# Kernel tuning notes

Measured on AMD Instinct MI355X. Metric: run time of the kernel, lower is better.

The kernel has to match this reference:

```python
import jax, jax.numpy as jnp
import numpy as np

N = 100000   # total nodes (batched molecules)
E = 250000   # directed edges
B = 2000     # number of graphs
F_IN = 75    # atom feature dim
DIM = 32     # hidden dim


def setup_inputs() -> dict:
    key = jax.random.key(0)
    ks = jax.random.split(key, 12)
    def gl(k, shape, fan_in):
        return (jax.random.normal(k, shape, jnp.float32) / np.sqrt(fan_in)).astype(jnp.float32)
    inp = {}
    inp['node_features'] = jax.random.normal(ks[0], (N, F_IN), jnp.float32)
    inp['edge_features'] = jax.random.normal(ks[1], (E, 11), jnp.float32)
    inp['lin0_w'] = gl(ks[2], (DIM, F_IN), F_IN)
    inp['lin0_b'] = jnp.zeros((DIM,), jnp.float32)
    # edge network: Linear(11,128) -> ReLU -> Linear(128, DIM*DIM)
    inp['nn_w1'] = gl(ks[3], (128, 11), 11)
    inp['nn_b1'] = jnp.zeros((128,), jnp.float32)
    inp['nn_w2'] = gl(ks[4], (DIM * DIM, 128), 128)
    inp['nn_b2'] = jnp.zeros((DIM * DIM,), jnp.float32)
    inp['conv_bias'] = jnp.zeros((DIM,), jnp.float32)  # NNConv bias (root_weight=False)
    # GRU(dim, dim), torch gate order: r, z, n
    inp['gru_wih'] = gl(ks[5], (3 * DIM, DIM), DIM)
    inp['gru_whh'] = gl(ks[6], (3 * DIM, DIM), DIM)
    inp['gru_bih'] = jnp.zeros((3 * DIM,), jnp.float32)
    inp['gru_bhh'] = jnp.zeros((3 * DIM,), jnp.float32)
    # Set2Set LSTM(2*dim, dim), torch gate order: i, f, g, o
    inp['lstm_wih'] = gl(ks[7], (4 * DIM, 2 * DIM), 2 * DIM)
    inp['lstm_whh'] = gl(ks[8], (4 * DIM, DIM), DIM)
    inp['lstm_bih'] = jnp.zeros((4 * DIM,), jnp.float32)
    inp['lstm_bhh'] = jnp.zeros((4 * DIM,), jnp.float32)
    inp['edge_index'] = jax.random.randint(ks[9], (2, E), 0, N)
    inp['graph_index'] = jnp.sort(jax.random.randint(ks[10], (N,), 0, B))
    return inp


def _nnconv(x, edge_w, src, dst, bias):
    # per-edge: gather src features, apply [dim,dim] edge weight, scatter-mean to dst
    msg = jnp.einsum('ei,eio->eo', x[src], edge_w)           # [E, DIM]
    s = jax.ops.segment_sum(msg, dst, num_segments=N)         # [N, DIM]
    cnt = jax.ops.segment_sum(jnp.ones((msg.shape[0],), msg.dtype), dst, num_segments=N)
    mean = s / jnp.maximum(cnt, 1.0)[:, None]
    return mean + bias


def _gru_cell(x, h, wih, whh, bih, bhh):
    gi = x @ wih.T + bih
    gh = h @ whh.T + bhh
    gi_r, gi_z, gi_n = jnp.split(gi, 3, axis=-1)
    gh_r, gh_z, gh_n = jnp.split(gh, 3, axis=-1)
    r = jax.nn.sigmoid(gi_r + gh_r)
    z = jax.nn.sigmoid(gi_z + gh_z)
    n = jnp.tanh(gi_n + r * gh_n)
    return (1.0 - z) * n + z * h


def _lstm_cell(x, h, c, wih, whh, bih, bhh):
    g = x @ wih.T + bih + h @ whh.T + bhh
    i, f, gg, o = jnp.split(g, 4, axis=-1)
    c = jax.nn.sigmoid(f) * c + jax.nn.sigmoid(i) * jnp.tanh(gg)
    h = jax.nn.sigmoid(o) * jnp.tanh(c)
    return h, c


def _set2set(x, batch, wih, whh, bih, bhh, steps=3):
    dim = x.shape[-1]
    h = jnp.zeros((B, dim), x.dtype)
    c = jnp.zeros((B, dim), x.dtype)
    q_star = jnp.zeros((B, 2 * dim), x.dtype)
    for _ in range(steps):
        q, c = _lstm_cell(q_star, h, c, wih, whh, bih, bhh)
        h = q
        e = jnp.sum(x * q[batch], axis=-1)                    # [N]
        emax = jax.ops.segment_max(e, batch, num_segments=B)
        ex = jnp.exp(e - emax[batch])
        denom = jax.ops.segment_sum(ex, batch, num_segments=B)
        a = ex / denom[batch]
        r = jax.ops.segment_sum(a[:, None] * x, batch, num_segments=B)
        q_star = jnp.concatenate([q, r], axis=-1)
    return q_star


def reference(node_features, edge_features, lin0_w, lin0_b, nn_w1, nn_b1, nn_w2, nn_b2,
              conv_bias, gru_wih, gru_whh, gru_bih, gru_bhh,
              lstm_wih, lstm_whh, lstm_bih, lstm_bhh, edge_index, graph_index):
    src, dst = edge_index[0], edge_index[1]
    out = jax.nn.relu(node_features @ lin0_w.T + lin0_b)      # [N, DIM]
    # edge network (edge_features are fixed -> identical every iteration)
    hw = jax.nn.relu(edge_features @ nn_w1.T + nn_b1)
    edge_w = (hw @ nn_w2.T + nn_b2).reshape(-1, DIM, DIM)     # [E, DIM, DIM]
    h = out
    for _ in range(3):
        m = jax.nn.relu(_nnconv(out, edge_w, src, dst, conv_bias))
        h = _gru_cell(m, h, gru_wih, gru_whh, gru_bih, gru_bhh)
        out = h
    pooled = _set2set(out, graph_index, lstm_wih, lstm_whh, lstm_bih, lstm_bhh)
    return pooled, out
```

## Files before the change

### kernel.cpp

```cpp
#include <hip/hip_runtime.h>
#include <stdint.h>

#define N_NODES  100000
#define N_EDGES  250000
#define N_GRAPHS 2000
#define F_IN     75
#define DIM      32
#define H1       128

#define MSG_BLOCKS 977
#define CH        8
#define NSTAGES   17
#define KT_PAD    (CH * NSTAGES)
#define W2F_HALFS (KT_PAD * 1024)

#define CNT_BLOCKS  ((N_EDGES + 255) / 256)
#define OFFS_BLOCKS ((N_NODES + 255) / 256)
#define GRUW_BLOCKS 32

typedef _Float16 v8h __attribute__((ext_vector_type(8)));
typedef float    v4f __attribute__((ext_vector_type(4)));

__device__ __forceinline__ void gld_lds16(const void* g, void* l) {
    __builtin_amdgcn_global_load_lds(
        (const __attribute__((address_space(1))) unsigned int*)g,
        (__attribute__((address_space(3))) unsigned int*)l, 16, 0, 0);
}

__global__ __launch_bounds__(256) void lin0_kernel(
    const float* __restrict__ nf, const float* __restrict__ w,
    const float* __restrict__ b, _Float16* __restrict__ h16) {
    __shared__ float wl[DIM * F_IN];
    __shared__ float bl[DIM];
    int t = threadIdx.x;
    for (int i = t; i < DIM * F_IN; i += 256) wl[i] = w[i];
    if (t < DIM) bl[t] = b[t];
    __syncthreads();
    int nl = t >> 5, o = t & 31;
    #pragma unroll
    for (int p = 0; p < 4; ++p) {
        int n = blockIdx.x * 32 + p * 8 + nl;
        if (n >= N_NODES) continue;
        const float* row = nf + (size_t)n * F_IN;
        float acc = bl[o];
        #pragma unroll
        for (int i = 0; i < F_IN; ++i) acc += row[i] * wl[o * F_IN + i];
        h16[(size_t)n * DIM + o] = (_Float16)fmaxf(acc, 0.f);
    }
}

__global__ __launch_bounds__(256) void prep_w2f_kernel(
    const float* __restrict__ w2, const float* __restrict__ b2,
    _Float16* __restrict__ w2f) {
    int id = blockIdx.x * 256 + threadIdx.x;
    if (id >= W2F_HALFS) return;
    int j    = id & 7;
    int lane = (id >> 3) & 63;
    int ng   = (id >> 9) & 1;
    int kt   = id >> 10;
    int lr = lane & 15, q = lane >> 4;
    int c = kt * 32 + q * 8 + j;
    int o = ng * 16 + lr;
    float val = 0.f;
    if (c < 4096)      val = w2[((c >> 7) * 32 + o) * H1 + (c & 127)];
    else if (c < 4128) val = b2[(c - 4096) * 32 + o];
    w2f[id] = (_Float16)val;
}

__global__ __launch_bounds__(256) void hw_kernel(
    const float* __restrict__ ef, const float* __restrict__ w1,
    const float* __restrict__ b1, _Float16* __restrict__ hwf,
    int e_off) {
    __shared__ float wl[H1 * 11];
    __shared__ float bl[H1];
    int t = threadIdx.x;
    for (int i = t; i < H1 * 11; i += 256) wl[i] = w1[i];
    if (t < H1) bl[t] = b1[t];
    __syncthreads();
    int k = t & 127;
    #pragma unroll
    for (int p = 0; p < 16; ++p) {
        int le = blockIdx.x * 32 + p * 2 + (t >> 7);
        int e  = e_off + le;
        float acc = 0.f;
        if (e < N_EDGES) {
            const float* row = ef + (size_t)e * 11;
            acc = bl[k];
            #pragma unroll
            for (int i = 0; i < 11; ++i) acc += row[i] * wl[k * 11 + i];
            acc = fmaxf(acc, 0.f);
        }
        size_t addr = (size_t)(le >> 4) * 2048 + (k >> 3) * 128 + (le & 15) * 8 + (k & 7);
        hwf[addr] = (_Float16)acc;
    }
}

__global__ __launch_bounds__(256) void aux_kernel(
    const int* __restrict__ dst, float* __restrict__ cnt,
    const int* __restrict__ gidx, int* __restrict__ gstart,
    const float* __restrict__ wih, const float* __restrict__ whh,
    _Float16* __restrict__ gw) {
    int t = threadIdx.x;
    if (blockIdx.x < CNT_BLOCKS) {
        int e = blockIdx.x * 256 + t;
        if (e < N_EDGES) atomicAdd(&cnt[dst[e]], 1.0f);
    } else if (blockIdx.x < CNT_BLOCKS + OFFS_BLOCKS) {
        int n = (blockIdx.x - CNT_BLOCKS) * 256 + t;
        if (n >= N_NODES) return;
        int b = gidx[n];
        if (n == 0) {
            for (int bb = 0; bb <= b; ++bb) gstart[bb] = 0;
        } else {
            int a = gidx[n - 1];
            for (int bb = a + 1; bb <= b; ++bb) gstart[bb] = n;
        }
        if (n == N_NODES - 1) {
            for (int bb = b + 1; bb <= N_GRAPHS; ++bb) gstart[bb] = N_NODES;
        }
    } else {
        int id = (blockIdx.x - CNT_BLOCKS - OFFS_BLOCKS) * 256 + t;
        if (id >= 8192) return;
        int im = id & 4095;
        int r = im / 40, c = im - r * 40;
        float val = 0.f;
        if (r < 96 && c < 32) val = (id < 4096) ? wih[r * 32 + c] : whh[r * 32 + c];
        gw[id] = (_Float16)val;
    }
}

__global__ __launch_bounds__(256) void msg_kernel(
    const _Float16* __restrict__ hwf, const _Float16* __restrict__ w2f,
    const _Float16* __restrict__ x16, const int* __restrict__ src,
    const int* __restrict__ dst, float* __restrict__ sbuf, int e_off) {
    __shared__ _Float16 xs[32 * 256];
    __shared__ _Float16 bst[2][CH * 1024];

    int t = threadIdx.x;
    int w = t >> 6, lane = t & 63, lr = lane & 15, q = lane >> 4;
    int wbase = w * 64;

    {
        const char* gp = (const char*)w2f;
        char* lp = (char*)&bst[0][0];
        #pragma unroll
        for (int it = 0; it < 4; ++it)
            gld_lds16(gp + it * 4096 + t * 16, lp + it * 4096 + t * 16);
    }

    v8h hwr[4][4];
    {
        const v8h* hv = (const v8h*)hwf;
        int T0 = blockIdx.x * 16 + w * 4;
        #pragma unroll
        for (int mt = 0; mt < 4; ++mt)
            #pragma unroll
            for (int kc = 0; kc < 4; ++kc)
                hwr[mt][kc] = hv[(size_t)(T0 + mt) * 256 + (kc * 4 + q) * 16 + lr];
    }

    {
        int e = e_off + blockIdx.x * 256 + t;
        int ec = e < N_EDGES ? e : N_EDGES - 1;
        int sv = src[ec];
        const v8h* xr = (const v8h*)(x16 + (size_t)sv * DIM);
        #pragma unroll
        for (int u = 0; u < 4; ++u) {
            v8h v = xr[u];
            #pragma unroll
            for (int j = 0; j < 8; ++j)
                xs[(u * 8 + j) * 256 + t] = v[j];
        }
    }
    __syncthreads();

    v4f acc[4][2];
    #pragma unroll
    for (int mt = 0; mt < 4; ++mt)
        #pragma unroll
        for (int ng = 0; ng < 2; ++ng) { v4f z = {0.f, 0.f, 0.f, 0.f}; acc[mt][ng] = z; }

    _Float16 xsc[4];

    for (int s = 0; s < NSTAGES - 1; ++s) {
        {
            const char* gp = (const char*)(w2f + (size_t)(s + 1) * CH * 1024);
            char* lp = (char*)&bst[(s + 1) & 1][0];
            #pragma unroll
            for (int it = 0; it < 4; ++it)
                gld_lds16(gp + it * 4096 + t * 16, lp + it * 4096 + t * 16);
        }
        const _Float16* bb = &bst[s & 1][0];
        #pragma unroll
        for (int ktl = 0; ktl < CH; ++ktl) {
            int kt = s * CH + ktl;
            v8h b0 = *(const v8h*)(bb + ktl * 1024 + lane * 8);
            v8h b1 = *(const v8h*)(bb + ktl * 1024 + 512 + lane * 8);
            if ((kt & 3) == 0) {
                int i = kt >> 2;
                #pragma unroll
                for (int mt = 0; mt < 4; ++mt)
                    xsc[mt] = xs[i * 256 + wbase + mt * 16 + lr];
            }
            int kc = kt & 3;
            #pragma unroll
            for (int mt = 0; mt < 4; ++mt) {
                v8h a = hwr[mt][kc] * xsc[mt];
                acc[mt][0] = __builtin_amdgcn_mfma_f32_16x16x32_f16(a, b0, acc[mt][0], 0, 0, 0);
                acc[mt][1] = __builtin_amdgcn_mfma_f32_16x16x32_f16(a, b1, acc[mt][1], 0, 0, 0);
            }
        }
        __syncthreads();
    }
    {
        const _Float16* bb = &bst[0][0];
        v8h b0 = *(const v8h*)(bb + lane * 8);
        v8h b1 = *(const v8h*)(bb + 512 + lane * 8);
        #pragma unroll
        for (int mt = 0; mt < 4; ++mt) {
            v8h a;
            #pragma unroll
            for (int j = 0; j < 8; ++j)
                a[j] = xs[(q * 8 + j) * 256 + wbase + mt * 16 + lr];
            acc[mt][0] = __builtin_amdgcn_mfma_f32_16x16x32_f16(a, b0, acc[mt][0], 0, 0, 0);
            acc[mt][1] = __builtin_amdgcn_mfma_f32_16x16x32_f16(a, b1, acc[mt][1], 0, 0, 0);
        }
    }

    int E0 = e_off + blockIdx.x * 256 + wbase;
    #pragma unroll
    for (int mt = 0; mt < 4; ++mt) {
        #pragma unroll
        for (int r = 0; r < 4; ++r) {
            int e = E0 + mt * 16 + q * 4 + r;
            if (e < N_EDGES) {
                int dv = dst[e];
                float* sp = sbuf + (size_t)dv * DIM;
                atomicAdd(sp + lr,      acc[mt][0][r]);
                atomicAdd(sp + 16 + lr, acc[mt][1][r]);
            }
        }
    }
}

__global__ __launch_bounds__(256) void gru_kernel(
    float* __restrict__ s, const float* __restrict__ cnt,
    const float* __restrict__ cb, const _Float16* __restrict__ gw,
    const float* __restrict__ bih, const float* __restrict__ bhh,
    _Float16* __restrict__ h16, float* __restrict__ hout, int last) {
    __shared__ _Float16 wi_l[4096], wh_l[4096];
    __shared__ float bi_l[96], bh_l[96];
    __shared__ _Float16 m_l[128 * 32], h_l[128 * 32];
    int t = threadIdx.x;

    {
        const char* gp = (const char*)gw;
        gld_lds16(gp + t * 16,         (char*)wi_l + t * 16);
        gld_lds16(gp + 4096 + t * 16,  (char*)wi_l + 4096 + t * 16);
        gld_lds16(gp + 8192 + t * 16,  (char*)wh_l + t * 16);
        gld_lds16(gp + 12288 + t * 16, (char*)wh_l + 4096 + t * 16);
    }
    if (t < 96) { bi_l[t] = bih[t]; bh_l[t] = bhh[t]; }

    {
        int node_l = t >> 1, part = t & 1;
        int n = blockIdx.x * 128 + node_l;
        int nc = n < N_NODES ? n : N_NODES - 1;
        float c = cnt[nc];
        float rc = 1.f / (c > 1.f ? c : 1.f);
        float4* s4 = (float4*)(s + (size_t)nc * DIM + part * 16);
        const float* cbp = cb + part * 16;
        #pragma unroll
        for (int u = 0; u < 2; ++u) {
            float4 sa = s4[u * 2], sb = s4[u * 2 + 1];
            v8h mv;
            mv[0] = (_Float16)fmaxf(sa.x * rc + cbp[u * 8 + 0], 0.f);
            mv[1] = (_Float16)fmaxf(sa.y * rc + cbp[u * 8 + 1], 0.f);
            mv[2] = (_Float16)fmaxf(sa.z * rc + cbp[u * 8 + 2], 0.f);
            mv[3] = (_Float16)fmaxf(sa.w * rc + cbp[u * 8 + 3], 0.f);
            mv[4] = (_Float16)fmaxf(sb.x * rc + cbp[u * 8 + 4], 0.f);
            mv[5] = (_Float16)fmaxf(sb.y * rc + cbp[u * 8 + 5], 0.f);
            mv[6] = (_Float16)fmaxf(sb.z * rc + cbp[u * 8 + 6], 0.f);
            mv[7] = (_Float16)fmaxf(sb.w * rc + cbp[u * 8 + 7], 0.f);
            *(v8h*)&m_l[node_l * 32 + part * 16 + u * 8] = mv;
        }
        if (n < N_NODES) {
            float4 z4 = {0.f, 0.f, 0.f, 0.f};
            s4[0] = z4; s4[1] = z4; s4[2] = z4; s4[3] = z4;
        }
        const v8h* h8 = (const v8h*)(h16 + (size_t)nc * DIM + part * 16);
        *(v8h*)&h_l[node_l * 32 + part * 16]     = h8[0];
        *(v8h*)&h_l[node_l * 32 + part * 16 + 8] = h8[1];
    }

    __syncthreads();

    int w = t >> 6, lane = t & 63, lr = lane & 15, q = lane >> 4;

    v8h bi6[6], bh6[6];
    #pragma unroll
    for (int nt = 0; nt < 6; ++nt) {
        bi6[nt] = *(const v8h*)&wi_l[(nt * 16 + lr) * 40 + q * 8];
        bh6[nt] = *(const v8h*)&wh_l[(nt * 16 + lr) * 40 + q * 8];
    }

    #pragma unroll
    for (int p = 0; p < 2; ++p) {
        int tb = w * 32 + p * 16;
        v4f ai[6], ah[6];
        #pragma unroll
        for (int nt = 0; nt < 6; ++nt) {
            float bii = bi_l[nt * 16 + lr], bhi = bh_l[nt * 16 + lr];
            v4f ci = {bii, bii, bii, bii}; ai[nt] = ci;
            v4f chh = {bhi, bhi, bhi, bhi}; ah[nt] = chh;
        }
        v8h ma = *(const v8h*)&m_l[(tb + lr) * 32 + q * 8];
        v8h ha = *(const v8h*)&h_l[(tb + lr) * 32 + q * 8];
        #pragma unroll
        for (int nt = 0; nt < 6; ++nt) {
            ai[nt] = __builtin_amdgcn_mfma_f32_16x16x32_f16(ma, bi6[nt], ai[nt], 0, 0, 0);
            ah[nt] = __builtin_amdgcn_mfma_f32_16x16x32_f16(ha, bh6[nt], ah[nt], 0, 0, 0);
        }
        int nb = blockIdx.x * 128 + tb + q * 4;
        #pragma unroll
        for (int g = 0; g < 2; ++g) {
            int o = g * 16 + lr;
            #pragma unroll
            for (int r = 0; r < 4; ++r) {
                int n2 = nb + r;
                if (n2 < N_NODES) {
                    float rg = 1.f / (1.f + expf(-(ai[g][r]     + ah[g][r])));
                    float zg = 1.f / (1.f + expf(-(ai[2 + g][r] + ah[2 + g][r])));
                    float ng = tanhf(ai[4 + g][r] + rg * ah[4 + g][r]);
                    float hold = (float)h_l[(tb + q * 4 + r) * 32 + o];
                    float hn = (1.f - zg) * ng + zg * hold;
                    h16[(size_t)n2 * DIM + o] = (_Float16)hn;
                    if (last) hout[(size_t)n2 * DIM + o] = hn;
                }
            }
        }
    }
}

__global__ __launch_bounds__(256) void s2s_kernel(
    const float* __restrict__ wih, const float* __restrict__ whh,
    const float* __restrict__ bih, const float* __restrict__ bhh,
    float* __restrict__ h, float* __restrict__ c,
    float* __restrict__ rnum, float* __restrict__ denom,
    const float* __restrict__ x, const int* __restrict__ gstart,
    float* __restrict__ outp, int first, int wout) {
    __shared__ float wA[128 * 33], wB[128 * 33], bl[128];
    int t = threadIdx.x;
    for (int i = t; i < 128 * 32; i += 256) {
        int r = i >> 5, cc = i & 31;
        wA[r * 33 + cc] = wih[r * 64 + cc] + whh[r * 32 + cc];
        wB[r * 33 + cc] = wih[r * 64 + 32 + cc];
    }
    if (t < 128) bl[t] = bih[t] + bhh[t];
    __syncthreads();
    int gl = t >> 5, o = t & 31;
    int b = blockIdx.x * 8 + gl;
    if (b >= N_GRAPHS) return;

    float hq = 0.f, rr = 0.f, cv = 0.f;
    if (!first) {
        hq = h[b * DIM + o];
        float d = denom[b];
        rr = d > 0.f ? rnum[b * DIM + o] / d : 0.f;
        cv = c[b * DIM + o];
    }
    float gi = bl[o], gf = bl[32 + o], gg = bl[64 + o], go = bl[96 + o];
    #pragma unroll
    for (int i = 0; i < 32; ++i) {
        float qv = __shfl(hq, i, 32);
        float rv = __shfl(rr, i, 32);
        gi += qv * wA[o * 33 + i]        + rv * wB[o * 33 + i];
        gf += qv * wA[(32 + o) * 33 + i] + rv * wB[(32 + o) * 33 + i];
        gg += qv * wA[(64 + o) * 33 + i] + rv * wB[(64 + o) * 33 + i];
        go += qv * wA[(96 + o) * 33 + i] + rv * wB[(96 + o) * 33 + i];
    }
    float si = 1.f / (1.f + expf(-gi));
    float sf = 1.f / (1.f + expf(-gf));
    float so = 1.f / (1.f + expf(-go));
    float cn = sf * cv + si * tanhf(gg);
    float qo = so * tanhf(cn);
    c[b * DIM + o] = cn;
    h[b * DIM + o] = qo;

    int n0 = gstart[b], n1 = gstart[b + 1];
    float m0 = -3.0e38f, s = 0.f, r = 0.f;
    for (int n = n0; n < n1; ++n) {
        float xo = x[(size_t)n * DIM + o];
        float e = xo * qo;
        #pragma unroll
        for (int mm = 16; mm >= 1; mm >>= 1) e += __shfl_xor(e, mm, 32);
        float nm = fmaxf(m0, e);
        float sc = expf(m0 - nm);
        float ex = expf(e - nm);
        s = s * sc + ex;
        r = r * sc + ex * xo;
        m0 = nm;
    }
    rnum[b * DIM + o] = r;
    if (o == 0) denom[b] = s;
    if (wout) {
        outp[b * 64 + o]      = qo;
        outp[b * 64 + 32 + o] = s > 0.f ? r / s : 0.f;
    }
}

extern "C" void kernel_launch(void* const* d_in, const int* in_sizes, int n_in,
                              void* d_out, int out_size, void* d_ws, size_t ws_size,
                              hipStream_t stream) {
    const float* nf   = (const float*)d_in[0];
    const float* ef   = (const float*)d_in[1];
    const float* l0w  = (const float*)d_in[2];
    const float* l0b  = (const float*)d_in[3];
    const float* w1   = (const float*)d_in[4];
    const float* b1   = (const float*)d_in[5];
    const float* w2   = (const float*)d_in[6];
    const float* b2   = (const float*)d_in[7];
    const float* cb   = (const float*)d_in[8];
    const float* gwih = (const float*)d_in[9];
    const float* gwhh = (const float*)d_in[10];
    const float* gbih = (const float*)d_in[11];
    const float* gbhh = (const float*)d_in[12];
    const float* lwih = (const float*)d_in[13];
    const float* lwhh = (const float*)d_in[14];
    const float* lbih = (const float*)d_in[15];
    const float* lbhh = (const float*)d_in[16];
    const int*   eidx = (const int*)d_in[17];
    const int*   gidx = (const int*)d_in[18];
    const int* src = eidx;
    const int* dst = eidx + N_EDGES;
    float* out = (float*)d_out;
    float* h   = out + (size_t)N_GRAPHS * 64;

    char* ws = (char*)d_ws;
    size_t off = 0;
    auto alloc = [&](size_t bytes) -> void* {
        void* p = ws + off;
        off = (off + bytes + 255) & ~(size_t)255;
        return p;
    };
    float* sbuf  = (float*)alloc((size_t)N_NODES * DIM * 4);
    float* cnt   = (float*)alloc((size_t)N_NODES * 4);
    _Float16* h16 = (_Float16*)alloc((size_t)N_NODES * DIM * 2);
    float* hs    = (float*)alloc((size_t)N_GRAPHS * DIM * 4);
    float* cs    = (float*)alloc((size_t)N_GRAPHS * DIM * 4);
    float* rnum  = (float*)alloc((size_t)N_GRAPHS * DIM * 4);
    float* denom = (float*)alloc((size_t)N_GRAPHS * 4);
    int*   gstart = (int*)alloc((size_t)(N_GRAPHS + 1) * 4);
    _Float16* w2f  = (_Float16*)alloc((size_t)W2F_HALFS * 2);
    _Float16* gw   = (_Float16*)alloc((size_t)16384);
    size_t fixed = off;
    size_t avail = ws_size > fixed ? ws_size - fixed : 0;

    auto need = [&](int nc) -> size_t {
        int cbk = (MSG_BLOCKS + nc - 1) / nc;
        return (size_t)cbk * 16 * 4096;
    };
    int nchunk = 1;
    while (nchunk < 64 && need(nchunk) > avail) nchunk <<= 1;
    int chunk_blocks = (MSG_BLOCKS + nchunk - 1) / nchunk;
    _Float16* hwf = (_Float16*)alloc(need(nchunk));

    lin0_kernel<<<dim3((N_NODES + 31) / 32), dim3(256), 0, stream>>>(nf, l0w, l0b, h16);
    prep_w2f_kernel<<<dim3((W2F_HALFS + 255) / 256), dim3(256), 0, stream>>>(w2, b2, w2f);
    hipMemsetAsync(cnt, 0, (size_t)N_NODES * 4, stream);
    aux_kernel<<<dim3(CNT_BLOCKS + OFFS_BLOCKS + GRUW_BLOCKS), dim3(256), 0, stream>>>(
        dst, cnt, gidx, gstart, gwih, gwhh, gw);
    if (nchunk == 1) {
        hw_kernel<<<dim3(MSG_BLOCKS * 8), dim3(256), 0, stream>>>(ef, w1, b1, hwf, 0);
    }
    hipMemsetAsync(sbuf, 0, (size_t)N_NODES * DIM * 4, stream);

    for (int it = 0; it < 3; ++it) {
        for (int cix = 0; cix < nchunk; ++cix) {
            int bstart = cix * chunk_blocks;
            int bc = MSG_BLOCKS - bstart;
            if (bc <= 0) break;
            if (bc > chunk_blocks) bc = chunk_blocks;
            int e_off = bstart * 256;
            if (nchunk > 1)
                hw_kernel<<<dim3(bc * 8), dim3(256), 0, stream>>>(ef, w1, b1, hwf, e_off);
            msg_kernel<<<dim3(bc), dim3(256), 0, stream>>>(hwf, w2f, h16, src, dst, sbuf, e_off);
        }
        gru_kernel<<<dim3((N_NODES + 127) / 128), dim3(256), 0, stream>>>(
            sbuf, cnt, cb, gw, gbih, gbhh, h16, h, it == 2 ? 1 : 0);
    }

    for (int st = 0; st < 3; ++st) {
        s2s_kernel<<<dim3((N_GRAPHS + 7) / 8), dim3(256), 0, stream>>>(
            lwih, lwhh, lbih, lbhh, hs, cs, rnum, denom, h, gstart, out,
            st == 0 ? 1 : 0, st == 2 ? 1 : 0);
    }
}
```

Before: 595.9 us.

## Fuse setup launches and run all Set2Set steps in one kernel

The memsets of cnt and sbuf are folded into lin0_kernel, and the w2f prep is merged into aux_kernel as extra blocks. This removes two memset calls and one kernel launch. The three Set2Set launches become a single kernel that loops over the steps and keeps the LSTM state and readout in registers, which drops the global h/c/rnum/denom round trips and two launches. The fused kernel reloads its weights only once, but it serializes the three steps inside each block.

```diff
diff --git a/kernel.cpp b/kernel.cpp
--- a/kernel.cpp
+++ b/kernel.cpp
@@ -17,6 +17,7 @@
 #define CNT_BLOCKS  ((N_EDGES + 255) / 256)
 #define OFFS_BLOCKS ((N_NODES + 255) / 256)
 #define GRUW_BLOCKS 32
+#define W2F_BLOCKS  ((W2F_HALFS + 255) / 256)
 
 typedef _Float16 v8h __attribute__((ext_vector_type(8)));
 typedef float    v4f __attribute__((ext_vector_type(4)));
@@ -29,7 +30,8 @@
 
 __global__ __launch_bounds__(256) void lin0_kernel(
     const float* __restrict__ nf, const float* __restrict__ w,
-    const float* __restrict__ b, _Float16* __restrict__ h16) {
+    const float* __restrict__ b, _Float16* __restrict__ h16,
+    float* __restrict__ cnt, float* __restrict__ sbuf) {
     __shared__ float wl[DIM * F_IN];
     __shared__ float bl[DIM];
     int t = threadIdx.x;
@@ -47,24 +49,65 @@
         for (int i = 0; i < F_IN; ++i) acc += row[i] * wl[o * F_IN + i];
         h16[(size_t)n * DIM + o] = (_Float16)fmaxf(acc, 0.f);
     }
-}
-
-__global__ __launch_bounds__(256) void prep_w2f_kernel(
+    if (t < 32) {
+        int n = blockIdx.x * 32 + t;
+        if (n < N_NODES) cnt[n] = 0.f;
+    }
+    #pragma unroll
+    for (int p = 0; p < 4; ++p) {
+        size_t idx = (size_t)blockIdx.x * 1024 + p * 256 + t;
+        if (idx < (size_t)N_NODES * DIM) sbuf[idx] = 0.f;
+    }
+}
+
+__global__ __launch_bounds__(256) void aux_kernel(
+    const int* __restrict__ dst, float* __restrict__ cnt,
+    const int* __restrict__ gidx, int* __restrict__ gstart,
+    const float* __restrict__ wih, const float* __restrict__ whh,
+    _Float16* __restrict__ gw,
     const float* __restrict__ w2, const float* __restrict__ b2,
     _Float16* __restrict__ w2f) {
-    int id = blockIdx.x * 256 + threadIdx.x;
-    if (id >= W2F_HALFS) return;
-    int j    = id & 7;
-    int lane = (id >> 3) & 63;
-    int ng   = (id >> 9) & 1;
-    int kt   = id >> 10;
-    int lr = lane & 15, q = lane >> 4;
-    int c = kt * 32 + q * 8 + j;
-    int o = ng * 16 + lr;
-    float val = 0.f;
-    if (c < 4096)      val = w2[((c >> 7) * 32 + o) * H1 + (c & 127)];
-    else if (c < 4128) val = b2[(c - 4096) * 32 + o];
-    w2f[id] = (_Float16)val;
+    int t = threadIdx.x;
+    unsigned bx = blockIdx.x;
+    if (bx < CNT_BLOCKS) {
+        int e = bx * 256 + t;
+        if (e < N_EDGES) atomicAdd(&cnt[dst[e]], 1.0f);
+    } else if (bx < CNT_BLOCKS + OFFS_BLOCKS) {
+        int n = (bx - CNT_BLOCKS) * 256 + t;
+        if (n >= N_NODES) return;
+        int b = gidx[n];
+        if (n == 0) {
+            for (int bb = 0; bb <= b; ++bb) gstart[bb] = 0;
+        } else {
+            int a = gidx[n - 1];
+            for (int bb = a + 1; bb <= b; ++bb) gstart[bb] = n;
+        }
+        if (n == N_NODES - 1) {
+            for (int bb = b + 1; bb <= N_GRAPHS; ++bb) gstart[bb] = N_NODES;
+        }
+    } else if (bx < CNT_BLOCKS + OFFS_BLOCKS + GRUW_BLOCKS) {
+        int id = (bx - CNT_BLOCKS - OFFS_BLOCKS) * 256 + t;
+        if (id >= 8192) return;
+        int im = id & 4095;
+        int r = im / 40, c = im - r * 40;
+        float val = 0.f;
+        if (r < 96 && c < 32) val = (id < 4096) ? wih[r * 32 + c] : whh[r * 32 + c];
+        gw[id] = (_Float16)val;
+    } else {
+        int id = (bx - CNT_BLOCKS - OFFS_BLOCKS - GRUW_BLOCKS) * 256 + t;
+        if (id >= W2F_HALFS) return;
+        int j    = id & 7;
+        int lane = (id >> 3) & 63;
+        int ng   = (id >> 9) & 1;
+        int kt   = id >> 10;
+        int lr = lane & 15, q = lane >> 4;
+        int c = kt * 32 + q * 8 + j;
+        int o = ng * 16 + lr;
+        float val = 0.f;
+        if (c < 4096)      val = w2[((c >> 7) * 32 + o) * H1 + (c & 127)];
+        else if (c < 4128) val = b2[(c - 4096) * 32 + o];
+        w2f[id] = (_Float16)val;
+    }
 }
 
 __global__ __launch_bounds__(256) void hw_kernel(
@@ -92,39 +135,6 @@
         }
         size_t addr = (size_t)(le >> 4) * 2048 + (k >> 3) * 128 + (le & 15) * 8 + (k & 7);
         hwf[addr] = (_Float16)acc;
-    }
-}
-
-__global__ __launch_bounds__(256) void aux_kernel(
-    const int* __restrict__ dst, float* __restrict__ cnt,
-    const int* __restrict__ gidx, int* __restrict__ gstart,
-    const float* __restrict__ wih, const float* __restrict__ whh,
-    _Float16* __restrict__ gw) {
-    int t = threadIdx.x;
-    if (blockIdx.x < CNT_BLOCKS) {
-        int e = blockIdx.x * 256 + t;
-        if (e < N_EDGES) atomicAdd(&cnt[dst[e]], 1.0f);
-    } else if (blockIdx.x < CNT_BLOCKS + OFFS_BLOCKS) {
-        int n = (blockIdx.x - CNT_BLOCKS) * 256 + t;
-        if (n >= N_NODES) return;
-        int b = gidx[n];
-        if (n == 0) {
-            for (int bb = 0; bb <= b; ++bb) gstart[bb] = 0;
-        } else {
-            int a = gidx[n - 1];
-            for (int bb = a + 1; bb <= b; ++bb) gstart[bb] = n;
-        }
-        if (n == N_NODES - 1) {
-            for (int bb = b + 1; bb <= N_GRAPHS; ++bb) gstart[bb] = N_NODES;
-        }
-    } else {
-        int id = (blockIdx.x - CNT_BLOCKS - OFFS_BLOCKS) * 256 + t;
-        if (id >= 8192) return;
-        int im = id & 4095;
-        int r = im / 40, c = im - r * 40;
-        float val = 0.f;
-        if (r < 96 && c < 32) val = (id < 4096) ? wih[r * 32 + c] : whh[r * 32 + c];
-        gw[id] = (_Float16)val;
     }
 }
 
@@ -344,10 +354,8 @@
 __global__ __launch_bounds__(256) void s2s_kernel(
     const float* __restrict__ wih, const float* __restrict__ whh,
     const float* __restrict__ bih, const float* __restrict__ bhh,
-    float* __restrict__ h, float* __restrict__ c,
-    float* __restrict__ rnum, float* __restrict__ denom,
     const float* __restrict__ x, const int* __restrict__ gstart,
-    float* __restrict__ outp, int first, int wout) {
+    float* __restrict__ outp) {
     __shared__ float wA[128 * 33], wB[128 * 33], bl[128];
     int t = threadIdx.x;
     for (int i = t; i < 128 * 32; i += 256) {
@@ -360,52 +368,44 @@
     int gl = t >> 5, o = t & 31;
     int b = blockIdx.x * 8 + gl;
     if (b >= N_GRAPHS) return;
+    int n0 = gstart[b], n1 = gstart[b + 1];
 
     float hq = 0.f, rr = 0.f, cv = 0.f;
-    if (!first) {
-        hq = h[b * DIM + o];
-        float d = denom[b];
-        rr = d > 0.f ? rnum[b * DIM + o] / d : 0.f;
-        cv = c[b * DIM + o];
-    }
-    float gi = bl[o], gf = bl[32 + o], gg = bl[64 + o], go = bl[96 + o];
-    #pragma unroll
-    for (int i = 0; i < 32; ++i) {
-        float qv = __shfl(hq, i, 32);
-        float rv = __shfl(rr, i, 32);
-        gi += qv * wA[o * 33 + i]        + rv * wB[o * 33 + i];
-        gf += qv * wA[(32 + o) * 33 + i] + rv * wB[(32 + o) * 33 + i];
-        gg += qv * wA[(64 + o) * 33 + i] + rv * wB[(64 + o) * 33 + i];
-        go += qv * wA[(96 + o) * 33 + i] + rv * wB[(96 + o) * 33 + i];
-    }
-    float si = 1.f / (1.f + expf(-gi));
-    float sf = 1.f / (1.f + expf(-gf));
-    float so = 1.f / (1.f + expf(-go));
-    float cn = sf * cv + si * tanhf(gg);
-    float qo = so * tanhf(cn);
-    c[b * DIM + o] = cn;
-    h[b * DIM + o] = qo;
-
-    int n0 = gstart[b], n1 = gstart[b + 1];
-    float m0 = -3.0e38f, s = 0.f, r = 0.f;
-    for (int n = n0; n < n1; ++n) {
-        float xo = x[(size_t)n * DIM + o];
-        float e = xo * qo;
-        #pragma unroll
-        for (int mm = 16; mm >= 1; mm >>= 1) e += __shfl_xor(e, mm, 32);
-        float nm = fmaxf(m0, e);
-        float sc = expf(m0 - nm);
-        float ex = expf(e - nm);
-        s = s * sc + ex;
-        r = r * sc + ex * xo;
-        m0 = nm;
-    }
-    rnum[b * DIM + o] = r;
-    if (o == 0) denom[b] = s;
-    if (wout) {
-        outp[b * 64 + o]      = qo;
-        outp[b * 64 + 32 + o] = s > 0.f ? r / s : 0.f;
-    }
+    #pragma unroll 1
+    for (int st = 0; st < 3; ++st) {
+        float gi = bl[o], gf = bl[32 + o], gg = bl[64 + o], go = bl[96 + o];
+        #pragma unroll
+        for (int i = 0; i < 32; ++i) {
+            float qv = __shfl(hq, i, 32);
+            float rv = __shfl(rr, i, 32);
+            gi += qv * wA[o * 33 + i]        + rv * wB[o * 33 + i];
+            gf += qv * wA[(32 + o) * 33 + i] + rv * wB[(32 + o) * 33 + i];
+            gg += qv * wA[(64 + o) * 33 + i] + rv * wB[(64 + o) * 33 + i];
+            go += qv * wA[(96 + o) * 33 + i] + rv * wB[(96 + o) * 33 + i];
+        }
+        float si = 1.f / (1.f + expf(-gi));
+        float sf = 1.f / (1.f + expf(-gf));
+        float so = 1.f / (1.f + expf(-go));
+        cv = sf * cv + si * tanhf(gg);
+        hq = so * tanhf(cv);
+
+        float m0 = -3.0e38f, s = 0.f, r = 0.f;
+        for (int n = n0; n < n1; ++n) {
+            float xo = x[(size_t)n * DIM + o];
+            float e = xo * hq;
+            #pragma unroll
+            for (int mm = 16; mm >= 1; mm >>= 1) e += __shfl_xor(e, mm, 32);
+            float nm = fmaxf(m0, e);
+            float sc = expf(m0 - nm);
+            float ex = expf(e - nm);
+            s = s * sc + ex;
+            r = r * sc + ex * xo;
+            m0 = nm;
+        }
+        rr = s > 0.f ? r / s : 0.f;
+    }
+    outp[b * 64 + o]      = hq;
+    outp[b * 64 + 32 + o] = rr;
 }
 
 extern "C" void kernel_launch(void* const* d_in, const int* in_sizes, int n_in,
@@ -445,10 +445,6 @@
     float* sbuf  = (float*)alloc((size_t)N_NODES * DIM * 4);
     float* cnt   = (float*)alloc((size_t)N_NODES * 4);
     _Float16* h16 = (_Float16*)alloc((size_t)N_NODES * DIM * 2);
-    float* hs    = (float*)alloc((size_t)N_GRAPHS * DIM * 4);
-    float* cs    = (float*)alloc((size_t)N_GRAPHS * DIM * 4);
-    float* rnum  = (float*)alloc((size_t)N_GRAPHS * DIM * 4);
-    float* denom = (float*)alloc((size_t)N_GRAPHS * 4);
     int*   gstart = (int*)alloc((size_t)(N_GRAPHS + 1) * 4);
     _Float16* w2f  = (_Float16*)alloc((size_t)W2F_HALFS * 2);
     _Float16* gw   = (_Float16*)alloc((size_t)16384);
@@ -464,15 +460,13 @@
     int chunk_blocks = (MSG_BLOCKS + nchunk - 1) / nchunk;
     _Float16* hwf = (_Float16*)alloc(need(nchunk));
 
-    lin0_kernel<<<dim3((N_NODES + 31) / 32), dim3(256), 0, stream>>>(nf, l0w, l0b, h16);
-    prep_w2f_kernel<<<dim3((W2F_HALFS + 255) / 256), dim3(256), 0, stream>>>(w2, b2, w2f);
-    hipMemsetAsync(cnt, 0, (size_t)N_NODES * 4, stream);
-    aux_kernel<<<dim3(CNT_BLOCKS + OFFS_BLOCKS + GRUW_BLOCKS), dim3(256), 0, stream>>>(
-        dst, cnt, gidx, gstart, gwih, gwhh, gw);
+    lin0_kernel<<<dim3((N_NODES + 31) / 32), dim3(256), 0, stream>>>(
+        nf, l0w, l0b, h16, cnt, sbuf);
+    aux_kernel<<<dim3(CNT_BLOCKS + OFFS_BLOCKS + GRUW_BLOCKS + W2F_BLOCKS), dim3(256), 0, stream>>>(
+        dst, cnt, gidx, gstart, gwih, gwhh, gw, w2, b2, w2f);
     if (nchunk == 1) {
         hw_kernel<<<dim3(MSG_BLOCKS * 8), dim3(256), 0, stream>>>(ef, w1, b1, hwf, 0);
     }
-    hipMemsetAsync(sbuf, 0, (size_t)N_NODES * DIM * 4, stream);
 
     for (int it = 0; it < 3; ++it) {
         for (int cix = 0; cix < nchunk; ++cix) {
@@ -489,9 +483,6 @@
             sbuf, cnt, cb, gw, gbih, gbhh, h16, h, it == 2 ? 1 : 0);
     }
 
-    for (int st = 0; st < 3; ++st) {
-        s2s_kernel<<<dim3((N_GRAPHS + 7) / 8), dim3(256), 0, stream>>>(
-            lwih, lwhh, lbih, lbhh, hs, cs, rnum, denom, h, gstart, out,
-            st == 0 ? 1 : 0, st == 2 ? 1 : 0);
-    }
-}
+    s2s_kernel<<<dim3((N_GRAPHS + 7) / 8), dim3(256), 0, stream>>>(
+        lwih, lwhh, lbih, lbhh, h, gstart, out);
+}
```

New measurement: 587.0 us. About the same (-1.5%).
